# Performance work log

Hardware: AMD Instinct MI355X
Metric: run time of the kernel (lower is better)

Reference implementation:

```python
import jax, jax.numpy as jnp
import numpy as np

N_EMBD = 512
N_HEAD = 8
HEAD_DIM = N_EMBD // N_HEAD


def setup_inputs() -> dict:
    key = jax.random.key(0)
    ks = jax.random.split(key, 10)
    B, Tx, Tc, C = 8, 1024, 2048, N_EMBD
    s = 1.0 / np.sqrt(C)
    return {
        "x": jax.random.normal(ks[0], (B, Tx, C), dtype=jnp.float32),
        "context": jax.random.normal(ks[1], (B, Tc, C), dtype=jnp.float32),
        "Wq": jax.random.normal(ks[2], (C, C), dtype=jnp.float32) * s,
        "bq": jnp.zeros((C,), dtype=jnp.float32),
        "Wk": jax.random.normal(ks[3], (C, C), dtype=jnp.float32) * s,
        "bk": jnp.zeros((C,), dtype=jnp.float32),
        "Wv": jax.random.normal(ks[4], (C, C), dtype=jnp.float32) * s,
        "bv": jnp.zeros((C,), dtype=jnp.float32),
        "Wo": jax.random.normal(ks[5], (C, C), dtype=jnp.float32) * s,
        "bo": jnp.zeros((C,), dtype=jnp.float32),
    }


def reference(x, context, Wq, bq, Wk, bk, Wv, bv, Wo, bo):
    B, Tx, C = x.shape
    Tc = context.shape[1]
    nh, hd = N_HEAD, C // N_HEAD
    # projections (torch Linear: y = x @ W.T + b)
    q = (x @ Wq.T + bq).reshape(B, Tx, nh, hd).transpose(0, 2, 1, 3)
    k = (context @ Wk.T + bk).reshape(B, Tc, nh, hd).transpose(0, 2, 1, 3)
    v = (context @ Wv.T + bv).reshape(B, Tc, nh, hd).transpose(0, 2, 1, 3)
    # attention scores (B, nh, Tx, Tc)
    att = jnp.einsum("bhqd,bhkd->bhqk", q, k) * (1.0 / np.sqrt(hd))
    att = jax.nn.softmax(att, axis=-1)
    y = jnp.einsum("bhqk,bhkd->bhqd", att, v)
    y = y.transpose(0, 2, 1, 3).reshape(B, Tx, C)
    att_mean = att.mean(axis=1)  # (B, Tx, Tc)
    y = y @ Wo.T + bo
    return (y, att_mean)
```

## Files before the change

### kernel.cpp

```cpp
#include <hip/hip_runtime.h>

#define DEVI __device__ __forceinline__

typedef short bf16x8 __attribute__((ext_vector_type(8)));
typedef short bf16x4 __attribute__((ext_vector_type(4)));
typedef float f32x4 __attribute__((ext_vector_type(4)));

constexpr int Bb = 8, TX = 1024, TC = 2048, CC = 512, NH = 8, HD = 64;
constexpr float LOG2E = 1.44269504f;

DEVI unsigned short f2bf(float f) {
  union { float f; unsigned u; } v; v.f = f;
  return (unsigned short)((v.u + 0x7FFFu + ((v.u >> 16) & 1u)) >> 16);
}

DEVI unsigned cvtpk(float lo, float hi) {
  unsigned r;
  asm("v_cvt_pk_bf16_f32 %0, %1, %2" : "=v"(r) : "v"(lo), "v"(hi));
  return r;
}

DEVI f32x4 mfma16(bf16x8 a, bf16x8 b, f32x4 c) {
  return __builtin_amdgcn_mfma_f32_16x16x32_bf16(a, b, c, 0, 0, 0);
}

DEVI f32x4 zero4() { f32x4 z = {0.f, 0.f, 0.f, 0.f}; return z; }

__global__ __launch_bounds__(256) void cvt_bf16(
    const float* __restrict__ src, unsigned short* __restrict__ dst, int n8) {
  int i = blockIdx.x * 256 + threadIdx.x;
  const int stride = gridDim.x * 256;
  for (; i < n8; i += stride) {
    f32x4 a = *(const f32x4*)(src + (size_t)i * 8);
    f32x4 b = *(const f32x4*)(src + (size_t)i * 8 + 4);
    bf16x8 v;
#pragma unroll
    for (int j = 0; j < 4; j++) {
      v[j] = (short)f2bf(a[j]);
      v[j + 4] = (short)f2bf(b[j]);
    }
    *(bf16x8*)(dst + (size_t)i * 8) = v;
  }
}

template <int MODE>
__global__ __launch_bounds__(256) void proj_gemm(
    const unsigned short* __restrict__ A, const unsigned short* __restrict__ W,
    const float* __restrict__ bias, void* __restrict__ outp, int tlog2, float scale) {
  __shared__ __align__(16) unsigned short As[64 * 40];
  __shared__ __align__(16) unsigned short Bs[64 * 40];

  const int tid = threadIdx.x;
  const int wid = tid >> 6, l = tid & 63, l15 = l & 15, lhi = l >> 4;
  const int wm = wid >> 1, wn = wid & 1;
  const int mbase = blockIdx.y * 64, nbase = blockIdx.x * 64;
  const int sr = tid >> 2, sc0 = (tid & 3) * 8;

  f32x4 acc[2][2];
#pragma unroll
  for (int i = 0; i < 2; i++)
#pragma unroll
    for (int j = 0; j < 2; j++) acc[i][j] = zero4();

  for (int k0 = 0; k0 < CC; k0 += 32) {
    *(bf16x8*)&As[sr * 40 + sc0] =
        *(const bf16x8*)(A + (size_t)(mbase + sr) * CC + k0 + sc0);
    *(bf16x8*)&Bs[sr * 40 + sc0] =
        *(const bf16x8*)(W + (size_t)(nbase + sr) * CC + k0 + sc0);
    __syncthreads();

    bf16x8 a0 = *(const bf16x8*)&As[(wm * 32 + l15) * 40 + lhi * 8];
    bf16x8 a1 = *(const bf16x8*)&As[(wm * 32 + 16 + l15) * 40 + lhi * 8];
    bf16x8 b0 = *(const bf16x8*)&Bs[(wn * 32 + l15) * 40 + lhi * 8];
    bf16x8 b1 = *(const bf16x8*)&Bs[(wn * 32 + 16 + l15) * 40 + lhi * 8];
    acc[0][0] = mfma16(a0, b0, acc[0][0]);
    acc[0][1] = mfma16(a0, b1, acc[0][1]);
    acc[1][0] = mfma16(a1, b0, acc[1][0]);
    acc[1][1] = mfma16(a1, b1, acc[1][1]);
    __syncthreads();
  }

#pragma unroll
  for (int mi = 0; mi < 2; mi++)
#pragma unroll
    for (int ni = 0; ni < 2; ni++)
#pragma unroll
      for (int r = 0; r < 4; r++) {
        int grow = mbase + wm * 32 + mi * 16 + 4 * lhi + r;
        int gcol = nbase + wn * 32 + ni * 16 + l15;
        float val = (acc[mi][ni][r] + bias[gcol]) * scale;
        if (MODE == 0) {
          int T = 1 << tlog2;
          int bq = grow >> tlog2, tt = grow & (T - 1);
          int h = gcol >> 6, d = gcol & 63;
          size_t oidx = ((size_t)(bq * NH + h) * T + tt) * HD + d;
          ((unsigned short*)outp)[oidx] = f2bf(val);
        } else {
          ((float*)outp)[(size_t)grow * CC + gcol] = val;
        }
      }
}

__global__ __launch_bounds__(256) void kv_gemm(
    const unsigned short* __restrict__ A, const unsigned short* __restrict__ Wk,
    const unsigned short* __restrict__ Wv, const float* __restrict__ bk,
    const float* __restrict__ bv, unsigned short* __restrict__ k_out,
    unsigned short* __restrict__ v_out) {
  __shared__ __align__(16) unsigned short As[64 * 40];
  __shared__ __align__(16) unsigned short Bks[64 * 40];
  __shared__ __align__(16) unsigned short Bvs[64 * 40];

  const int tid = threadIdx.x;
  const int wid = tid >> 6, l = tid & 63, l15 = l & 15, lhi = l >> 4;
  const int wm = wid >> 1, wn = wid & 1;
  const int mbase = blockIdx.y * 64, nbase = blockIdx.x * 64;
  const int sr = tid >> 2, sc0 = (tid & 3) * 8;

  f32x4 acck[2][2], accv[2][2];
#pragma unroll
  for (int i = 0; i < 2; i++)
#pragma unroll
    for (int j = 0; j < 2; j++) { acck[i][j] = zero4(); accv[i][j] = zero4(); }

  for (int k0 = 0; k0 < CC; k0 += 32) {
    *(bf16x8*)&As[sr * 40 + sc0] =
        *(const bf16x8*)(A + (size_t)(mbase + sr) * CC + k0 + sc0);
    *(bf16x8*)&Bks[sr * 40 + sc0] =
        *(const bf16x8*)(Wk + (size_t)(nbase + sr) * CC + k0 + sc0);
    *(bf16x8*)&Bvs[sr * 40 + sc0] =
        *(const bf16x8*)(Wv + (size_t)(nbase + sr) * CC + k0 + sc0);
    __syncthreads();

    bf16x8 a0 = *(const bf16x8*)&As[(wm * 32 + l15) * 40 + lhi * 8];
    bf16x8 a1 = *(const bf16x8*)&As[(wm * 32 + 16 + l15) * 40 + lhi * 8];
    bf16x8 k0f = *(const bf16x8*)&Bks[(wn * 32 + l15) * 40 + lhi * 8];
    bf16x8 k1f = *(const bf16x8*)&Bks[(wn * 32 + 16 + l15) * 40 + lhi * 8];
    bf16x8 v0f = *(const bf16x8*)&Bvs[(wn * 32 + l15) * 40 + lhi * 8];
    bf16x8 v1f = *(const bf16x8*)&Bvs[(wn * 32 + 16 + l15) * 40 + lhi * 8];
    acck[0][0] = mfma16(a0, k0f, acck[0][0]);
    acck[0][1] = mfma16(a0, k1f, acck[0][1]);
    acck[1][0] = mfma16(a1, k0f, acck[1][0]);
    acck[1][1] = mfma16(a1, k1f, acck[1][1]);
    accv[0][0] = mfma16(a0, v0f, accv[0][0]);
    accv[0][1] = mfma16(a0, v1f, accv[0][1]);
    accv[1][0] = mfma16(a1, v0f, accv[1][0]);
    accv[1][1] = mfma16(a1, v1f, accv[1][1]);
    __syncthreads();
  }

#pragma unroll
  for (int mi = 0; mi < 2; mi++)
#pragma unroll
    for (int ni = 0; ni < 2; ni++)
#pragma unroll
      for (int r = 0; r < 4; r++) {
        int grow = mbase + wm * 32 + mi * 16 + 4 * lhi + r;
        int gcol = nbase + wn * 32 + ni * 16 + l15;
        int bq = grow >> 11, tt = grow & (TC - 1);
        int h = gcol >> 6, d = gcol & 63;
        float kv = acck[mi][ni][r] + bk[gcol];
        float vv = accv[mi][ni][r] + bv[gcol];
        k_out[((size_t)(bq * NH + h) * TC + tt) * HD + d] = f2bf(kv);
        v_out[((size_t)(bq * NH + h) * HD + d) * TC + tt] = f2bf(vv);
      }
}

__global__ __launch_bounds__(512) void attn_fwd(
    const unsigned short* __restrict__ Qw, const unsigned short* __restrict__ Kw,
    const unsigned short* __restrict__ Vtw, unsigned short* __restrict__ y_pre,
    float* __restrict__ m_ws, float* __restrict__ il_ws) {
  __shared__ __align__(16) unsigned short ktl[2][64 * 64];
  __shared__ __align__(16) unsigned short vtl[2][64 * 64];

  const int tid = threadIdx.x;
  const int wid = tid >> 6, l = tid & 63, l15 = l & 15, lhi = l >> 4;
  const int qg = blockIdx.x, h = blockIdx.y, b = blockIdx.z;
  const int qbase = qg * 128 + wid * 16;

  const unsigned short* Qh = Qw + (size_t)(b * NH + h) * TX * HD;
  const unsigned short* Kh = Kw + (size_t)(b * NH + h) * TC * HD;
  const unsigned short* Vt = Vtw + (size_t)(b * NH + h) * TC * HD;

  bf16x8 aq0 = *(const bf16x8*)(Qh + (size_t)(qbase + l15) * HD + lhi * 8);
  bf16x8 aq1 = *(const bf16x8*)(Qh + (size_t)(qbase + l15) * HD + 32 + lhi * 8);

  f32x4 accy[4];
#pragma unroll
  for (int db = 0; db < 4; db++) accy[db] = zero4();
  float mrun = -1e30f, lrun = 0.f;

  const int sl0 = l15 + ((lhi & 1) << 5);
  const int sl1 = sl0 + 16;
  const bool sel = ((lhi >> 1) & 1) != 0;

  const int rs0 = (lhi ^ (l15 & 7)) << 3;
  const int rs1 = ((lhi ^ 4) ^ (l15 & 7)) << 3;

  const int sr = tid >> 3;
  const int ssw = ((tid & 7) ^ (sr & 7)) << 3;
  const int sc0 = (tid & 7) * 8;

  bf16x8 kr = *(const bf16x8*)(Kh + (size_t)sr * HD + sc0);
  bf16x8 vp = *(const bf16x8*)(Vt + (size_t)sr * TC + sc0);
  *(bf16x8*)&ktl[0][sr * 64 + ssw] = kr;
  *(bf16x8*)&vtl[0][sr * 64 + ssw] = vp;
  __syncthreads();

  constexpr int NT = TC / 64;
  for (int kt = 0; kt < NT; kt++) {
    const int cur = kt & 1;

    if (kt + 1 < NT) {
      const int keyn = (kt + 1) * 64;
      kr = *(const bf16x8*)(Kh + (size_t)(keyn + sr) * HD + sc0);
      vp = *(const bf16x8*)(Vt + (size_t)sr * TC + keyn + sc0);
    }

    f32x4 s[4];
    __builtin_amdgcn_s_setprio(1);
#pragma unroll
    for (int kb = 0; kb < 4; kb++) {
      bf16x8 bk0 = *(const bf16x8*)&ktl[cur][(kb * 16 + l15) * 64 + rs0];
      bf16x8 bk1 = *(const bf16x8*)&ktl[cur][(kb * 16 + l15) * 64 + rs1];
      f32x4 a = zero4();
      a = mfma16(bk0, aq0, a);
      a = mfma16(bk1, aq1, a);
      s[kb] = a;
    }
    __builtin_amdgcn_s_setprio(0);

    float mx = s[0][0];
#pragma unroll
    for (int kb = 0; kb < 4; kb++)
#pragma unroll
      for (int r = 0; r < 4; r++) mx = fmaxf(mx, s[kb][r]);
    mx = fmaxf(mx, __shfl_xor(mx, 16));
    mx = fmaxf(mx, __shfl_xor(mx, 32));

    if (__any(mx - mrun > 7.0f)) {
      float mn = fmaxf(mrun, mx);
      float sc = exp2f(mrun - mn);
      lrun *= sc;
      mrun = mn;
#pragma unroll
      for (int db = 0; db < 4; db++)
#pragma unroll
        for (int r = 0; r < 4; r++) accy[db][r] *= sc;
    }

    float p[4][4];
    float ps = 0.f;
#pragma unroll
    for (int kb = 0; kb < 4; kb++)
#pragma unroll
      for (int r = 0; r < 4; r++) {
        p[kb][r] = exp2f(s[kb][r] - mrun);
        ps += p[kb][r];
      }
    ps += __shfl_xor(ps, 16);
    ps += __shfl_xor(ps, 32);
    lrun += ps;

    unsigned pkw[4][2];
#pragma unroll
    for (int kb = 0; kb < 4; kb++) {
      pkw[kb][0] = cvtpk(p[kb][0], p[kb][1]);
      pkw[kb][1] = cvtpk(p[kb][2], p[kb][3]);
    }
    unsigned a00 = (unsigned)__shfl((int)pkw[0][0], sl0);
    unsigned a01 = (unsigned)__shfl((int)pkw[0][1], sl0);
    unsigned a10 = (unsigned)__shfl((int)pkw[1][0], sl0);
    unsigned a11 = (unsigned)__shfl((int)pkw[1][1], sl0);
    unsigned c00 = (unsigned)__shfl((int)pkw[0][0], sl1);
    unsigned c01 = (unsigned)__shfl((int)pkw[0][1], sl1);
    unsigned c10 = (unsigned)__shfl((int)pkw[1][0], sl1);
    unsigned c11 = (unsigned)__shfl((int)pkw[1][1], sl1);
    unsigned e00 = (unsigned)__shfl((int)pkw[2][0], sl0);
    unsigned e01 = (unsigned)__shfl((int)pkw[2][1], sl0);
    unsigned e10 = (unsigned)__shfl((int)pkw[3][0], sl0);
    unsigned e11 = (unsigned)__shfl((int)pkw[3][1], sl0);
    unsigned g00 = (unsigned)__shfl((int)pkw[2][0], sl1);
    unsigned g01 = (unsigned)__shfl((int)pkw[2][1], sl1);
    unsigned g10 = (unsigned)__shfl((int)pkw[3][0], sl1);
    unsigned g11 = (unsigned)__shfl((int)pkw[3][1], sl1);
    union { unsigned u[4]; bf16x8 v; } B0, B1;
    B0.u[0] = sel ? a10 : a00;
    B0.u[1] = sel ? a11 : a01;
    B0.u[2] = sel ? c10 : c00;
    B0.u[3] = sel ? c11 : c01;
    B1.u[0] = sel ? e10 : e00;
    B1.u[1] = sel ? e11 : e01;
    B1.u[2] = sel ? g10 : g00;
    B1.u[3] = sel ? g11 : g01;

    __builtin_amdgcn_s_setprio(1);
#pragma unroll
    for (int db = 0; db < 4; db++) {
      bf16x8 bv0 = *(const bf16x8*)&vtl[cur][(db * 16 + l15) * 64 + rs0];
      bf16x8 bv1 = *(const bf16x8*)&vtl[cur][(db * 16 + l15) * 64 + rs1];
      accy[db] = mfma16(bv0, B0.v, accy[db]);
      accy[db] = mfma16(bv1, B1.v, accy[db]);
    }
    __builtin_amdgcn_s_setprio(0);

    if (kt + 1 < NT) {
      const int nxt = cur ^ 1;
      *(bf16x8*)&ktl[nxt][sr * 64 + ssw] = kr;
      *(bf16x8*)&vtl[nxt][sr * 64 + ssw] = vp;
    }
    __syncthreads();
  }

  const float il = 1.f / lrun;

#pragma unroll
  for (int db = 0; db < 4; db++) {
    bf16x4 o;
#pragma unroll
    for (int r = 0; r < 4; r++) o[r] = (short)f2bf(accy[db][r] * il);
    *(bf16x4*)(y_pre + (size_t)(b * TX + qbase + l15) * CC + h * HD + db * 16 +
               4 * lhi) = o;
  }
  if (lhi == 0) {
    int idx = (b * NH + h) * TX + qbase + l15;
    m_ws[idx] = mrun;
    il_ws[idx] = il;
  }
}

__global__ __launch_bounds__(512) void att_mean_k(
    const unsigned short* __restrict__ Qw, const unsigned short* __restrict__ Kw,
    const float* __restrict__ m_ws, const float* __restrict__ il_ws,
    float* __restrict__ attm) {
  __shared__ __align__(16) unsigned short ktl[2][64 * 64];

  const int tid = threadIdx.x;
  const int wid = tid >> 6, l = tid & 63, l15 = l & 15, lhi = l >> 4;
  const int qbase = blockIdx.x * 128 + wid * 16;
  const int keyb = blockIdx.y * 64;
  const int b = blockIdx.z;

  const unsigned short* Qb = Qw + (size_t)b * NH * TX * HD;
  const unsigned short* Kb = Kw + (size_t)b * NH * TC * HD;

  const int rs0 = (lhi ^ (l15 & 7)) << 3;
  const int rs1 = ((lhi ^ 4) ^ (l15 & 7)) << 3;

  const int sr = tid >> 3;
  const int ssw = ((tid & 7) ^ (sr & 7)) << 3;
  const int sc0 = (tid & 7) * 8;

  bf16x8 aq0[2], aq1[2];
  f32x4 mm[2], ii[2];

  auto load_q = [&](int h, int p) {
    const unsigned short* qp =
        Qb + ((size_t)h * TX + qbase + l15) * HD + lhi * 8;
    aq0[p] = *(const bf16x8*)qp;
    aq1[p] = *(const bf16x8*)(qp + 32);
    mm[p] = *(const f32x4*)(m_ws + (size_t)(b * NH + h) * TX + qbase + 4 * lhi);
    ii[p] = *(const f32x4*)(il_ws + (size_t)(b * NH + h) * TX + qbase + 4 * lhi);
  };

  bf16x8 kr = *(const bf16x8*)(Kb + ((size_t)keyb + sr) * HD + sc0);
  load_q(0, 0);
  *(bf16x8*)&ktl[0][sr * 64 + ssw] = kr;
  __syncthreads();

  f32x4 am[4];
#pragma unroll
  for (int kb = 0; kb < 4; kb++) am[kb] = zero4();

#pragma unroll
  for (int h = 0; h < NH; h++) {
    const int cur = h & 1;

    if (h + 1 < NH) {
      kr = *(const bf16x8*)(Kb + ((size_t)(h + 1) * TC + keyb + sr) * HD + sc0);
      load_q(h + 1, cur ^ 1);
    }

#pragma unroll
    for (int kb = 0; kb < 4; kb++) {
      bf16x8 bk0 = *(const bf16x8*)&ktl[cur][(kb * 16 + l15) * 64 + rs0];
      bf16x8 bk1 = *(const bf16x8*)&ktl[cur][(kb * 16 + l15) * 64 + rs1];
      f32x4 a = zero4();
      a = mfma16(aq0[cur], bk0, a);
      a = mfma16(aq1[cur], bk1, a);
#pragma unroll
      for (int r = 0; r < 4; r++)
        am[kb][r] += exp2f(a[r] - mm[cur][r]) * ii[cur][r];
    }

    if (h + 1 < NH) {
      const int nxt = cur ^ 1;
      *(bf16x8*)&ktl[nxt][sr * 64 + ssw] = kr;
    }
    __syncthreads();
  }

#pragma unroll
  for (int kb = 0; kb < 4; kb++)
#pragma unroll
    for (int r = 0; r < 4; r++) {
      int trow = qbase + 4 * lhi + r;
      attm[(size_t)(b * TX + trow) * TC + keyb + kb * 16 + l15] = am[kb][r] * 0.125f;
    }
}

extern "C" void kernel_launch(void* const* d_in, const int* in_sizes, int n_in,
                              void* d_out, int out_size, void* d_ws, size_t ws_size,
                              hipStream_t stream) {
  const float* x   = (const float*)d_in[0];
  const float* ctx = (const float*)d_in[1];
  const float* Wq  = (const float*)d_in[2];
  const float* bq  = (const float*)d_in[3];
  const float* Wk  = (const float*)d_in[4];
  const float* bk  = (const float*)d_in[5];
  const float* Wv  = (const float*)d_in[6];
  const float* bv  = (const float*)d_in[7];
  const float* Wo  = (const float*)d_in[8];
  const float* bo  = (const float*)d_in[9];

  float* y_out = (float*)d_out;
  float* attm  = y_out + (size_t)Bb * TX * CC;

  unsigned short* q_ws = (unsigned short*)d_ws;
  unsigned short* k_ws = q_ws + (size_t)Bb * NH * TX * HD;
  unsigned short* v_ws = k_ws + (size_t)Bb * NH * TC * HD;
  float* m_ws  = (float*)(v_ws + (size_t)Bb * NH * TC * HD);
  float* il_ws = m_ws + (size_t)Bb * NH * TX;
  unsigned short* y_pre = (unsigned short*)(il_ws + (size_t)Bb * NH * TX);
  unsigned short* wb = y_pre + (size_t)Bb * TX * CC;
  unsigned short* wbq = wb, *wbk = wb + CC * CC, *wbv = wb + 2 * CC * CC,
                 *wbo = wb + 3 * CC * CC;

  unsigned short* xb = k_ws;
  unsigned short* cb = (unsigned short*)attm;

  const int NX8 = Bb * TX * CC / 8, NC8 = Bb * TC * CC / 8, NW8 = CC * CC / 8;
  cvt_bf16<<<dim3(2048), 256, 0, stream>>>(x, xb, NX8);
  cvt_bf16<<<dim3(2048), 256, 0, stream>>>(ctx, cb, NC8);
  cvt_bf16<<<dim3(128), 256, 0, stream>>>(Wq, wbq, NW8);
  cvt_bf16<<<dim3(128), 256, 0, stream>>>(Wk, wbk, NW8);
  cvt_bf16<<<dim3(128), 256, 0, stream>>>(Wv, wbv, NW8);
  cvt_bf16<<<dim3(128), 256, 0, stream>>>(Wo, wbo, NW8);

  proj_gemm<0><<<dim3(CC / 64, (Bb * TX) / 64), 256, 0, stream>>>(
      xb, wbq, bq, q_ws, 10, 0.125f * LOG2E);
  kv_gemm<<<dim3(CC / 64, (Bb * TC) / 64), 256, 0, stream>>>(cb, wbk, wbv, bk, bv, k_ws, v_ws);
  attn_fwd<<<dim3(TX / 128, NH, Bb), 512, 0, stream>>>(q_ws, k_ws, v_ws, y_pre, m_ws, il_ws);
  att_mean_k<<<dim3(TX / 128, TC / 64, Bb), 512, 0, stream>>>(q_ws, k_ws, m_ws, il_ws, attm);
  proj_gemm<1><<<dim3(CC / 64, (Bb * TX) / 64), 256, 0, stream>>>(y_pre, wbo, bo, y_out, 10, 1.0f);
}
```

Baseline: 229.0 us.

## Rewrite projection GEMMs with 128x128 tiles, double-buffered direct-to-LDS loads, XOR swizzle

```diff
diff --git a/kernel.cpp b/kernel.cpp
--- a/kernel.cpp
+++ b/kernel.cpp
@@ -25,6 +25,12 @@
 }
 
 DEVI f32x4 zero4() { f32x4 z = {0.f, 0.f, 0.f, 0.f}; return z; }
+
+DEVI void gload_lds16(const unsigned short* g, unsigned short* l) {
+  __builtin_amdgcn_global_load_lds(
+      (const __attribute__((address_space(1))) void*)g,
+      (__attribute__((address_space(3))) void*)l, 16, 0, 0);
+}
 
 __global__ __launch_bounds__(256) void cvt_bf16(
     const float* __restrict__ src, unsigned short* __restrict__ dst, int n8) {
@@ -44,50 +50,67 @@
 }
 
 template <int MODE>
-__global__ __launch_bounds__(256) void proj_gemm(
+__global__ __launch_bounds__(256, 3) void gemm128(
     const unsigned short* __restrict__ A, const unsigned short* __restrict__ W,
     const float* __restrict__ bias, void* __restrict__ outp, int tlog2, float scale) {
-  __shared__ __align__(16) unsigned short As[64 * 40];
-  __shared__ __align__(16) unsigned short Bs[64 * 40];
+  __shared__ __align__(16) unsigned short As[2][128 * 32];
+  __shared__ __align__(16) unsigned short Bs[2][128 * 32];
 
   const int tid = threadIdx.x;
   const int wid = tid >> 6, l = tid & 63, l15 = l & 15, lhi = l >> 4;
   const int wm = wid >> 1, wn = wid & 1;
-  const int mbase = blockIdx.y * 64, nbase = blockIdx.x * 64;
-  const int sr = tid >> 2, sc0 = (tid & 3) * 8;
-
-  f32x4 acc[2][2];
-#pragma unroll
-  for (int i = 0; i < 2; i++)
-#pragma unroll
-    for (int j = 0; j < 2; j++) acc[i][j] = zero4();
-
-  for (int k0 = 0; k0 < CC; k0 += 32) {
-    *(bf16x8*)&As[sr * 40 + sc0] =
-        *(const bf16x8*)(A + (size_t)(mbase + sr) * CC + k0 + sc0);
-    *(bf16x8*)&Bs[sr * 40 + sc0] =
-        *(const bf16x8*)(W + (size_t)(nbase + sr) * CC + k0 + sc0);
+  const int mbase = blockIdx.y * 128, nbase = blockIdx.x * 128;
+
+  f32x4 acc[4][4];
+#pragma unroll
+  for (int i = 0; i < 4; i++)
+#pragma unroll
+    for (int j = 0; j < 4; j++) acc[i][j] = zero4();
+
+  auto stage = [&](int buf, int k0) {
+#pragma unroll
+    for (int i = 0; i < 2; i++) {
+      const int u = wid * 128 + i * 64 + l;
+      const int row = u >> 2;
+      const int gc = ((u & 3) ^ ((row >> 1) & 3)) * 8;
+      const int lo = (wid * 128 + i * 64) * 8;
+      gload_lds16(A + (size_t)(mbase + row) * CC + k0 + gc, &As[buf][lo]);
+      gload_lds16(W + (size_t)(nbase + row) * CC + k0 + gc, &Bs[buf][lo]);
+    }
+  };
+
+  stage(0, 0);
+
+  const int sA = (lhi ^ ((l15 >> 1) & 3)) << 3;
+
+  constexpr int NK = CC / 32;
+  for (int kt = 0; kt < NK; kt++) {
+    const int cur = kt & 1;
     __syncthreads();
-
-    bf16x8 a0 = *(const bf16x8*)&As[(wm * 32 + l15) * 40 + lhi * 8];
-    bf16x8 a1 = *(const bf16x8*)&As[(wm * 32 + 16 + l15) * 40 + lhi * 8];
-    bf16x8 b0 = *(const bf16x8*)&Bs[(wn * 32 + l15) * 40 + lhi * 8];
-    bf16x8 b1 = *(const bf16x8*)&Bs[(wn * 32 + 16 + l15) * 40 + lhi * 8];
-    acc[0][0] = mfma16(a0, b0, acc[0][0]);
-    acc[0][1] = mfma16(a0, b1, acc[0][1]);
-    acc[1][0] = mfma16(a1, b0, acc[1][0]);
-    acc[1][1] = mfma16(a1, b1, acc[1][1]);
-    __syncthreads();
-  }
-
-#pragma unroll
-  for (int mi = 0; mi < 2; mi++)
-#pragma unroll
-    for (int ni = 0; ni < 2; ni++)
+    if (kt + 1 < NK) stage(cur ^ 1, (kt + 1) * 32);
+
+    bf16x8 af[4], bfr[4];
+#pragma unroll
+    for (int mi = 0; mi < 4; mi++)
+      af[mi] = *(const bf16x8*)&As[cur][(wm * 64 + mi * 16 + l15) * 32 + sA];
+#pragma unroll
+    for (int ni = 0; ni < 4; ni++)
+      bfr[ni] = *(const bf16x8*)&Bs[cur][(wn * 64 + ni * 16 + l15) * 32 + sA];
+#pragma unroll
+    for (int mi = 0; mi < 4; mi++)
+#pragma unroll
+      for (int ni = 0; ni < 4; ni++)
+        acc[mi][ni] = mfma16(af[mi], bfr[ni], acc[mi][ni]);
+  }
+
+#pragma unroll
+  for (int mi = 0; mi < 4; mi++)
+#pragma unroll
+    for (int ni = 0; ni < 4; ni++)
 #pragma unroll
       for (int r = 0; r < 4; r++) {
-        int grow = mbase + wm * 32 + mi * 16 + 4 * lhi + r;
-        int gcol = nbase + wn * 32 + ni * 16 + l15;
+        int grow = mbase + wm * 64 + mi * 16 + 4 * lhi + r;
+        int gcol = nbase + wn * 64 + ni * 16 + l15;
         float val = (acc[mi][ni][r] + bias[gcol]) * scale;
         if (MODE == 0) {
           int T = 1 << tlog2;
@@ -101,61 +124,75 @@
       }
 }
 
-__global__ __launch_bounds__(256) void kv_gemm(
+__global__ __launch_bounds__(256, 2) void kv_gemm128(
     const unsigned short* __restrict__ A, const unsigned short* __restrict__ Wk,
     const unsigned short* __restrict__ Wv, const float* __restrict__ bk,
     const float* __restrict__ bv, unsigned short* __restrict__ k_out,
     unsigned short* __restrict__ v_out) {
-  __shared__ __align__(16) unsigned short As[64 * 40];
-  __shared__ __align__(16) unsigned short Bks[64 * 40];
-  __shared__ __align__(16) unsigned short Bvs[64 * 40];
+  __shared__ __align__(16) unsigned short As[2][128 * 32];
+  __shared__ __align__(16) unsigned short Bks[2][128 * 32];
+  __shared__ __align__(16) unsigned short Bvs[2][128 * 32];
 
   const int tid = threadIdx.x;
   const int wid = tid >> 6, l = tid & 63, l15 = l & 15, lhi = l >> 4;
   const int wm = wid >> 1, wn = wid & 1;
-  const int mbase = blockIdx.y * 64, nbase = blockIdx.x * 64;
-  const int sr = tid >> 2, sc0 = (tid & 3) * 8;
-
-  f32x4 acck[2][2], accv[2][2];
-#pragma unroll
-  for (int i = 0; i < 2; i++)
-#pragma unroll
-    for (int j = 0; j < 2; j++) { acck[i][j] = zero4(); accv[i][j] = zero4(); }
-
-  for (int k0 = 0; k0 < CC; k0 += 32) {
-    *(bf16x8*)&As[sr * 40 + sc0] =
-        *(const bf16x8*)(A + (size_t)(mbase + sr) * CC + k0 + sc0);
-    *(bf16x8*)&Bks[sr * 40 + sc0] =
-        *(const bf16x8*)(Wk + (size_t)(nbase + sr) * CC + k0 + sc0);
-    *(bf16x8*)&Bvs[sr * 40 + sc0] =
-        *(const bf16x8*)(Wv + (size_t)(nbase + sr) * CC + k0 + sc0);
+  const int mbase = blockIdx.y * 128, nbase = blockIdx.x * 128;
+
+  f32x4 acck[4][4], accv[4][4];
+#pragma unroll
+  for (int i = 0; i < 4; i++)
+#pragma unroll
+    for (int j = 0; j < 4; j++) { acck[i][j] = zero4(); accv[i][j] = zero4(); }
+
+  auto stage = [&](int buf, int k0) {
+#pragma unroll
+    for (int i = 0; i < 2; i++) {
+      const int u = wid * 128 + i * 64 + l;
+      const int row = u >> 2;
+      const int gc = ((u & 3) ^ ((row >> 1) & 3)) * 8;
+      const int lo = (wid * 128 + i * 64) * 8;
+      gload_lds16(A + (size_t)(mbase + row) * CC + k0 + gc, &As[buf][lo]);
+      gload_lds16(Wk + (size_t)(nbase + row) * CC + k0 + gc, &Bks[buf][lo]);
+      gload_lds16(Wv + (size_t)(nbase + row) * CC + k0 + gc, &Bvs[buf][lo]);
+    }
+  };
+
+  stage(0, 0);
+
+  const int sA = (lhi ^ ((l15 >> 1) & 3)) << 3;
+
+  constexpr int NK = CC / 32;
+  for (int kt = 0; kt < NK; kt++) {
+    const int cur = kt & 1;
     __syncthreads();
-
-    bf16x8 a0 = *(const bf16x8*)&As[(wm * 32 + l15) * 40 + lhi * 8];
-    bf16x8 a1 = *(const bf16x8*)&As[(wm * 32 + 16 + l15) * 40 + lhi * 8];
-    bf16x8 k0f = *(const bf16x8*)&Bks[(wn * 32 + l15) * 40 + lhi * 8];
-    bf16x8 k1f = *(const bf16x8*)&Bks[(wn * 32 + 16 + l15) * 40 + lhi * 8];
-    bf16x8 v0f = *(const bf16x8*)&Bvs[(wn * 32 + l15) * 40 + lhi * 8];
-    bf16x8 v1f = *(const bf16x8*)&Bvs[(wn * 32 + 16 + l15) * 40 + lhi * 8];
-    acck[0][0] = mfma16(a0, k0f, acck[0][0]);
-    acck[0][1] = mfma16(a0, k1f, acck[0][1]);
-    acck[1][0] = mfma16(a1, k0f, acck[1][0]);
-    acck[1][1] = mfma16(a1, k1f, acck[1][1]);
-    accv[0][0] = mfma16(a0, v0f, accv[0][0]);
-    accv[0][1] = mfma16(a0, v1f, accv[0][1]);
-    accv[1][0] = mfma16(a1, v0f, accv[1][0]);
-    accv[1][1] = mfma16(a1, v1f, accv[1][1]);
-    __syncthreads();
-  }
-
-#pragma unroll
-  for (int mi = 0; mi < 2; mi++)
-#pragma unroll
-    for (int ni = 0; ni < 2; ni++)
+    if (kt + 1 < NK) stage(cur ^ 1, (kt + 1) * 32);
+
+    bf16x8 af[4], kf[4], vf[4];
+#pragma unroll
+    for (int mi = 0; mi < 4; mi++)
+      af[mi] = *(const bf16x8*)&As[cur][(wm * 64 + mi * 16 + l15) * 32 + sA];
+#pragma unroll
+    for (int ni = 0; ni < 4; ni++) {
+      kf[ni] = *(const bf16x8*)&Bks[cur][(wn * 64 + ni * 16 + l15) * 32 + sA];
+      vf[ni] = *(const bf16x8*)&Bvs[cur][(wn * 64 + ni * 16 + l15) * 32 + sA];
+    }
+#pragma unroll
+    for (int mi = 0; mi < 4; mi++)
+#pragma unroll
+      for (int ni = 0; ni < 4; ni++) {
+        acck[mi][ni] = mfma16(af[mi], kf[ni], acck[mi][ni]);
+        accv[mi][ni] = mfma16(af[mi], vf[ni], accv[mi][ni]);
+      }
+  }
+
+#pragma unroll
+  for (int mi = 0; mi < 4; mi++)
+#pragma unroll
+    for (int ni = 0; ni < 4; ni++)
 #pragma unroll
       for (int r = 0; r < 4; r++) {
-        int grow = mbase + wm * 32 + mi * 16 + 4 * lhi + r;
-        int gcol = nbase + wn * 32 + ni * 16 + l15;
+        int grow = mbase + wm * 64 + mi * 16 + 4 * lhi + r;
+        int gcol = nbase + wn * 64 + ni * 16 + l15;
         int bq = grow >> 11, tt = grow & (TC - 1);
         int h = gcol >> 6, d = gcol & 63;
         float kv = acck[mi][ni][r] + bk[gcol];
@@ -446,10 +483,12 @@
   cvt_bf16<<<dim3(128), 256, 0, stream>>>(Wv, wbv, NW8);
   cvt_bf16<<<dim3(128), 256, 0, stream>>>(Wo, wbo, NW8);
 
-  proj_gemm<0><<<dim3(CC / 64, (Bb * TX) / 64), 256, 0, stream>>>(
+  gemm128<0><<<dim3(CC / 128, (Bb * TX) / 128), 256, 0, stream>>>(
       xb, wbq, bq, q_ws, 10, 0.125f * LOG2E);
-  kv_gemm<<<dim3(CC / 64, (Bb * TC) / 64), 256, 0, stream>>>(cb, wbk, wbv, bk, bv, k_ws, v_ws);
+  kv_gemm128<<<dim3(CC / 128, (Bb * TC) / 128), 256, 0, stream>>>(
+      cb, wbk, wbv, bk, bv, k_ws, v_ws);
   attn_fwd<<<dim3(TX / 128, NH, Bb), 512, 0, stream>>>(q_ws, k_ws, v_ws, y_pre, m_ws, il_ws);
   att_mean_k<<<dim3(TX / 128, TC / 64, Bb), 512, 0, stream>>>(q_ws, k_ws, m_ws, il_ws, attm);
-  proj_gemm<1><<<dim3(CC / 64, (Bb * TX) / 64), 256, 0, stream>>>(y_pre, wbo, bo, y_out, 10, 1.0f);
-}
+  gemm128<1><<<dim3(CC / 128, (Bb * TX) / 128), 256, 0, stream>>>(
+      y_pre, wbo, bo, y_out, 10, 1.0f);
+}
```

Result: faster. 216.1 us (-5.6%).
